# Optimization experiments

Hardware: AMD Instinct MI355X
Metric: run time of the kernel (lower is better)

The kernel has to match this reference:

```python
import jax, jax.numpy as jnp
import numpy as np

B, S, D = 8, 2048, 512

def setup_inputs() -> dict:
    key = jax.random.key(0)
    ks = jax.random.split(key, 9)
    scale = 1.0 / np.sqrt(D)
    q = jax.random.normal(ks[0], (B, S, D), dtype=jnp.float32)
    k = jax.random.normal(ks[1], (B, S, D), dtype=jnp.float32)
    v = jax.random.normal(ks[2], (B, S, D), dtype=jnp.float32)
    # causal mask, broadcast over batch: True = attend
    mask = jnp.tril(jnp.ones((S, S), dtype=bool))[None, :, :]
    Wq = jax.random.normal(ks[3], (D, D), dtype=jnp.float32) * scale
    bq = jax.random.normal(ks[4], (D,), dtype=jnp.float32) * scale
    Wk = jax.random.normal(ks[5], (D, D), dtype=jnp.float32) * scale
    bk = jax.random.normal(ks[6], (D,), dtype=jnp.float32) * scale
    Wv = jax.random.normal(ks[7], (D, D), dtype=jnp.float32) * scale
    bv = jax.random.normal(ks[8], (D,), dtype=jnp.float32) * scale
    return {"q": q, "k": k, "v": v, "mask": mask,
            "Wq": Wq, "bq": bq, "Wk": Wk, "bk": bk, "Wv": Wv, "bv": bv}

def reference(q, k, v, mask, Wq, bq, Wk, bk, Wv, bv):
    # torch nn.Linear: x @ W^T + b
    Q = jnp.einsum('bsd,ed->bse', q, Wq) + bq
    K = jnp.einsum('bsd,ed->bse', k, Wk) + bk
    V = jnp.einsum('bsd,ed->bse', v, Wv) + bv
    scores = jnp.einsum('bqd,bkd->bqk', Q, K) / jnp.sqrt(jnp.float32(D))
    scores = jnp.where(mask, scores, jnp.float32(-1e9))
    prob = jax.nn.softmax(scores, axis=-1)
    out = jnp.einsum('bqk,bkd->bqd', prob, V)
    return out
```

## Files before the change

### kernel.cpp

```cpp
#include <hip/hip_runtime.h>
#include <stdint.h>
#include <stddef.h>
#include <math.h>

typedef _Float16 half8 __attribute__((ext_vector_type(8)));
typedef float f32x4 __attribute__((ext_vector_type(4)));

#define SCALE_QK 0.04419417382415922f

__device__ __forceinline__ void gload16(const void* g, void* lds) {
  __builtin_amdgcn_global_load_lds(
      (const __attribute__((address_space(1))) void*)g,
      (__attribute__((address_space(3))) void*)lds,
      16, 0, 0);
}

template<bool A_F32>
__device__ __forceinline__ void run_kloop(const void* Arow0, const _Float16* Brow0,
                                          int lda, int ldb, int kIters,
                                          _Float16* As0, _Float16* As1,
                                          _Float16* Bs0, _Float16* Bs1,
                                          f32x4 (&acc)[4][4])
{
  const int tid  = threadIdx.x;
  const int lane = tid & 63;
  const int w    = tid >> 6;
  const int wm   = w >> 1, wn = w & 1;
  const int srow = tid >> 3;
  const int sg   = tid & 7;
  const int swz  = sg ^ (srow & 7);
  const int fr   = lane & 15;
  const int fq   = lane >> 4;
  const int fx   = lane & 7;

  f32x4 preF[8];

  auto loadAreg = [&](int it) {
    const float* A = (const float*)Arow0;
    const int k0 = it * 64;
    #pragma unroll
    for (int i = 0; i < 4; ++i) {
      const float* src = A + (size_t)(i*32 + srow) * lda + (k0 + sg*8);
      preF[2*i]   = *(const f32x4*)src;
      preF[2*i+1] = *(const f32x4*)(src + 4);
    }
  };
  auto writeA = [&](_Float16* dst) {
    #pragma unroll
    for (int i = 0; i < 4; ++i) {
      f32x4 x = preF[2*i], y = preF[2*i+1];
      half8 h;
      h[0]=(_Float16)x[0]; h[1]=(_Float16)x[1]; h[2]=(_Float16)x[2]; h[3]=(_Float16)x[3];
      h[4]=(_Float16)y[0]; h[5]=(_Float16)y[1]; h[6]=(_Float16)y[2]; h[7]=(_Float16)y[3];
      *(half8*)(dst + (i*32 + srow)*64 + swz*8) = h;
    }
  };
  auto gloadA = [&](int it, _Float16* dst) {
    const _Float16* A = (const _Float16*)Arow0;
    const int k0 = it * 64;
    #pragma unroll
    for (int i = 0; i < 4; ++i)
      gload16(A + (size_t)(i*32 + srow) * lda + (k0 + swz*8), dst + i*2048 + w*512);
  };
  auto gloadB = [&](int it, _Float16* dst) {
    const int k0 = it * 64;
    #pragma unroll
    for (int i = 0; i < 4; ++i)
      gload16(Brow0 + (size_t)(i*32 + srow) * ldb + (k0 + swz*8), dst + i*2048 + w*512);
  };
  auto stage = [&](int it, _Float16* dA, _Float16* dB) {
    if constexpr (A_F32) loadAreg(it);
    else                 gloadA(it, dA);
    gloadB(it, dB);
  };
  auto compute = [&](const _Float16* cAs, const _Float16* cBs) {
    #pragma unroll
    for (int ks = 0; ks < 2; ++ks) {
      half8 av[4], bv[4];
      const int slot = (ks*4 + fq) ^ fx;
      #pragma unroll
      for (int i = 0; i < 4; ++i) {
        av[i] = *(const half8*)(cAs + (wm*64 + i*16 + fr)*64 + slot*8);
        bv[i] = *(const half8*)(cBs + (wn*64 + i*16 + fr)*64 + slot*8);
      }
      #pragma unroll
      for (int i = 0; i < 4; ++i) {
        #pragma unroll
        for (int j = 0; j < 4; ++j)
          acc[i][j] = __builtin_amdgcn_mfma_f32_16x16x32_f16(av[i], bv[j], acc[i][j], 0, 0, 0);
      }
    }
  };

  stage(0, As0, Bs0);
  if constexpr (A_F32) writeA(As0);
  __syncthreads();

  for (int it = 0; it < kIters; it += 2) {
    stage(it + 1, As1, Bs1);
    compute(As0, Bs0);
    if constexpr (A_F32) writeA(As1);
    __syncthreads();
    const bool more = (it + 2) < kIters;
    if (more) stage(it + 2, As0, Bs0);
    compute(As1, Bs1);
    if constexpr (A_F32) { if (more) writeA(As0); }
    __syncthreads();
  }
}

__global__ __launch_bounds__(256) void k_cvtw(const float* __restrict__ Wq,
                                              const float* __restrict__ Wk,
                                              const float* __restrict__ Wv,
                                              _Float16* __restrict__ Wb)
{
  const int t = blockIdx.x * 256 + threadIdx.x;
  const int base = t * 8;
  const int z = base >> 18;
  const int off = base & 262143;
  const float* src = (z == 0) ? Wq : ((z == 1) ? Wk : Wv);
  f32x4 a = *(const f32x4*)(src + off);
  f32x4 b = *(const f32x4*)(src + off + 4);
  half8 h;
  h[0]=(_Float16)a[0]; h[1]=(_Float16)a[1]; h[2]=(_Float16)a[2]; h[3]=(_Float16)a[3];
  h[4]=(_Float16)b[0]; h[5]=(_Float16)b[1]; h[6]=(_Float16)b[2]; h[7]=(_Float16)b[3];
  *(half8*)(Wb + base) = h;
}

__global__ __launch_bounds__(256) void k_proj(const float* __restrict__ q,
                                              const float* __restrict__ k,
                                              const float* __restrict__ v,
                                              const _Float16* __restrict__ Wb,
                                              const float* __restrict__ bq,
                                              const float* __restrict__ bk,
                                              const float* __restrict__ bv,
                                              _Float16* __restrict__ Qb,
                                              _Float16* __restrict__ Kb,
                                              _Float16* __restrict__ Vb)
{
  __shared__ __align__(16) _Float16 As0[128*64], As1[128*64];
  __shared__ __align__(16) _Float16 Bs0[128*64], Bs1[128*64];
  const int bid = blockIdx.x;
  const int xcd = bid & 7, i = bid >> 3;
  const int p = xcd * 48 + (i >> 2);
  const int nt = i & 3;
  const int z = p >> 7, mt = p & 127;

  const float* A     = (z == 0) ? q  : (z == 1) ? k  : v;
  const float* bia   = (z == 0) ? bq : (z == 1) ? bk : bv;
  const _Float16* B  = Wb + (size_t)z * 512 * 512;
  _Float16* C        = (z == 0) ? Qb : (z == 1) ? Kb : Vb;

  f32x4 acc[4][4] = {};
  run_kloop<true>(A + (size_t)mt*128*512, B + (size_t)nt*128*512, 512, 512, 8,
                  As0, As1, Bs0, Bs1, acc);

  const int lane = threadIdx.x & 63, w = threadIdx.x >> 6;
  const int wm = w >> 1, wn = w & 1;
  const int fr = lane & 15, fq = lane >> 4;
  #pragma unroll
  for (int j = 0; j < 4; ++j) {
    const int col = nt*128 + wn*64 + j*16 + fr;
    const float bval = bia[col];
    #pragma unroll
    for (int i2 = 0; i2 < 4; ++i2) {
      const int row = mt*128 + wm*64 + i2*16 + fq*4;
      #pragma unroll
      for (int r = 0; r < 4; ++r)
        C[(size_t)(row + r) * 512 + col] = (_Float16)(acc[i2][j][r] + bval);
    }
  }
}

__global__ __launch_bounds__(256) void k_trans(const _Float16* __restrict__ Vb,
                                               _Float16* __restrict__ Vt)
{
  __shared__ __align__(16) _Float16 t[64][72];
  const int st = blockIdx.x, dt = blockIdx.y, b = blockIdx.z;
  const int r = threadIdx.x >> 2, g = threadIdx.x & 3;
  const _Float16* src = Vb + ((size_t)b*2048 + st*64 + r)*512 + dt*64 + g*16;
  half8 v0 = *(const half8*)src;
  half8 v1 = *(const half8*)(src + 8);
  *(half8*)&t[r][g*16]     = v0;
  *(half8*)&t[r][g*16 + 8] = v1;
  __syncthreads();
  half8 o0, o1;
  #pragma unroll
  for (int i2 = 0; i2 < 8; ++i2) o0[i2] = t[g*16 + i2][r];
  #pragma unroll
  for (int i2 = 0; i2 < 8; ++i2) o1[i2] = t[g*16 + 8 + i2][r];
  _Float16* dst = Vt + ((size_t)b*512 + dt*64 + r)*2048 + st*64 + g*16;
  *(half8*)dst       = o0;
  *(half8*)(dst + 8) = o1;
}

__global__ __launch_bounds__(256) void k_scores(const _Float16* __restrict__ Qb,
                                                const _Float16* __restrict__ Kb,
                                                _Float16* __restrict__ P)
{
  const int bid = blockIdx.x;
  const int b = bid & 7;
  const int t = bid >> 3;
  int qt = (int)((sqrtf(8.0f * (float)t + 1.0f) - 1.0f) * 0.5f);
  int base = (qt * (qt + 1)) >> 1;
  if (t < base)                { --qt; base = (qt * (qt + 1)) >> 1; }
  else if (t >= base + qt + 1) { ++qt; base = (qt * (qt + 1)) >> 1; }
  const int kt = t - base;

  __shared__ __align__(16) _Float16 As0[128*64], As1[128*64];
  __shared__ __align__(16) _Float16 Bs0[128*64], Bs1[128*64];
  f32x4 acc[4][4] = {};
  run_kloop<false>(Qb + ((size_t)b*2048 + qt*128)*512,
                   Kb + ((size_t)b*2048 + kt*128)*512,
                   512, 512, 8, As0, As1, Bs0, Bs1, acc);
  const int lane = threadIdx.x & 63, w = threadIdx.x >> 6;
  const int wm = w >> 1, wn = w & 1;
  const int fr = lane & 15, fq = lane >> 4;
  #pragma unroll
  for (int i = 0; i < 4; ++i) {
    const int row = qt*128 + wm*64 + i*16 + fq*4;
    #pragma unroll
    for (int j = 0; j < 4; ++j) {
      const int col = kt*128 + wn*64 + j*16 + fr;
      #pragma unroll
      for (int r = 0; r < 4; ++r)
        P[((size_t)b*2048 + row + r) * 2048 + col] = (_Float16)(acc[i][j][r] * SCALE_QK);
    }
  }
}

__global__ __launch_bounds__(256) void k_softmax(_Float16* __restrict__ P)
{
  const int lane = threadIdx.x & 63;
  const int row  = blockIdx.x * 4 + (threadIdx.x >> 6);
  const int qIdx = row & 2047;
  _Float16* p = P + (size_t)row * 2048;
  const int L    = qIdx + 1;
  const int Lpad = ((qIdx >> 7) + 1) * 128;

  half8 xb[4];
  float m = -1e30f, s = 0.f;
  #pragma unroll
  for (int c = 0; c < 4; ++c) {
    const int i0 = lane * 8 + c * 512;
    if (i0 < Lpad) {
      half8 x = *(const half8*)(p + i0);
      xb[c] = x;
      float xv[8];
      #pragma unroll
      for (int j = 0; j < 8; ++j) xv[j] = (i0 + j < L) ? (float)x[j] : -1e30f;
      float cm = xv[0];
      #pragma unroll
      for (int j = 1; j < 8; ++j) cm = fmaxf(cm, xv[j]);
      const float mn = fmaxf(m, cm);
      float cs = 0.f;
      #pragma unroll
      for (int j = 0; j < 8; ++j) cs += __expf(xv[j] - mn);
      s = s * __expf(m - mn) + cs;
      m = mn;
    }
  }
  #pragma unroll
  for (int d = 1; d < 64; d <<= 1) {
    const float mo = __shfl_xor(m, d, 64);
    const float so = __shfl_xor(s, d, 64);
    const float mn = fmaxf(m, mo);
    s = s * __expf(m - mn) + so * __expf(mo - mn);
    m = mn;
  }
  const float inv = 1.0f / s;

  #pragma unroll
  for (int c = 0; c < 4; ++c) {
    const int i0 = lane * 8 + c * 512;
    if (i0 < Lpad) {
      half8 x = xb[c];
      half8 o;
      #pragma unroll
      for (int j = 0; j < 8; ++j)
        o[j] = (i0 + j < L) ? (_Float16)(__expf((float)x[j] - m) * inv) : (_Float16)0.f;
      *(half8*)(p + i0) = o;
    }
  }
}

__global__ __launch_bounds__(256) void k_pv(const _Float16* __restrict__ P,
                                            const _Float16* __restrict__ Vt,
                                            float* __restrict__ Out)
{
  const int bid = blockIdx.x;
  const int b = bid & 7;
  const int r0 = bid >> 3;
  const int qi = r0 >> 2, dt = r0 & 3;
  const int qt = (qi & 1) ? (15 - (qi >> 1)) : (qi >> 1);

  __shared__ __align__(16) _Float16 As0[128*64], As1[128*64];
  __shared__ __align__(16) _Float16 Bs0[128*64], Bs1[128*64];
  f32x4 acc[4][4] = {};
  run_kloop<false>(P  + ((size_t)b*2048 + qt*128)*2048,
                   Vt + ((size_t)b*512  + dt*128)*2048,
                   2048, 2048, (qt + 1) * 2, As0, As1, Bs0, Bs1, acc);
  const int lane = threadIdx.x & 63, w = threadIdx.x >> 6;
  const int wm = w >> 1, wn = w & 1;
  const int fr = lane & 15, fq = lane >> 4;
  #pragma unroll
  for (int i = 0; i < 4; ++i) {
    const int row = qt*128 + wm*64 + i*16 + fq*4;
    #pragma unroll
    for (int j = 0; j < 4; ++j) {
      const int col = dt*128 + wn*64 + j*16 + fr;
      #pragma unroll
      for (int r = 0; r < 4; ++r)
        Out[((size_t)b*2048 + row + r) * 512 + col] = acc[i][j][r];
    }
  }
}

extern "C" void kernel_launch(void* const* d_in, const int* in_sizes, int n_in,
                              void* d_out, int out_size, void* d_ws, size_t ws_size,
                              hipStream_t stream) {
  (void)in_sizes; (void)n_in; (void)out_size;
  const float* q  = (const float*)d_in[0];
  const float* k  = (const float*)d_in[1];
  const float* v  = (const float*)d_in[2];
  const float* Wq = (const float*)d_in[4];
  const float* bq = (const float*)d_in[5];
  const float* Wk = (const float*)d_in[6];
  const float* bk = (const float*)d_in[7];
  const float* Wv = (const float*)d_in[8];
  const float* bv = (const float*)d_in[9];

  const size_t OFF_P  = 0;
  const size_t OFF_Q  = (size_t)64 << 20;
  const size_t OFF_K  = (size_t)80 << 20;
  const size_t OFF_V  = (size_t)96 << 20;
  const size_t OFF_VT = (size_t)112 << 20;
  const size_t OFF_W  = (size_t)128 << 20;
  const size_t NEEDED = OFF_W + (size_t)3 * 512 * 512 * sizeof(_Float16);
  if (ws_size < NEEDED) return;

  char* ws = (char*)d_ws;
  _Float16* P  = (_Float16*)(ws + OFF_P);
  _Float16* Qb = (_Float16*)(ws + OFF_Q);
  _Float16* Kb = (_Float16*)(ws + OFF_K);
  _Float16* Vb = (_Float16*)(ws + OFF_V);
  _Float16* Vt = (_Float16*)(ws + OFF_VT);
  _Float16* Wb = (_Float16*)(ws + OFF_W);
  float* Out = (float*)d_out;

  k_cvtw   <<<dim3(384),      dim3(256), 0, stream>>>(Wq, Wk, Wv, Wb);
  k_proj   <<<dim3(1536),     dim3(256), 0, stream>>>(q, k, v, Wb, bq, bk, bv, Qb, Kb, Vb);
  k_trans  <<<dim3(32, 8, 8), dim3(256), 0, stream>>>(Vb, Vt);
  k_scores <<<dim3(1088),     dim3(256), 0, stream>>>(Qb, Kb, P);
  k_softmax<<<dim3(4096),     dim3(256), 0, stream>>>(P);
  k_pv     <<<dim3(512),      dim3(256), 0, stream>>>(P, Vt, Out);
}
```

Measured before the change: 272.5 us.

## Deepen GEMM k-loop prefetch using explicit vmcnt waits and raw barriers

Restructures the double-buffered k-loop so two stages are in flight at once. It replaces __syncthreads with raw s_barrier plus explicit s_waitcnt vmcnt/lgkmcnt counts, so the current tile's loads are waited on while the next tile's loads stay outstanding. The aim is to hide global-load latency behind MFMA compute. In exchange it adds more barriers per iteration, and correctness now depends on hand-counted vmcnt values matching the number of issued loads.

```diff
diff --git a/kernel.cpp b/kernel.cpp
--- a/kernel.cpp
+++ b/kernel.cpp
@@ -7,6 +7,11 @@
 typedef float f32x4 __attribute__((ext_vector_type(4)));
 
 #define SCALE_QK 0.04419417382415922f
+
+#define WAITVM(N) asm volatile("s_waitcnt vmcnt(" #N ")" ::: "memory")
+#define WAITLG0() asm volatile("s_waitcnt lgkmcnt(0)" ::: "memory")
+#define BAR()     __builtin_amdgcn_s_barrier()
+#define SCHED0()  __builtin_amdgcn_sched_barrier(0)
 
 __device__ __forceinline__ void gload16(const void* g, void* lds) {
   __builtin_amdgcn_global_load_lds(
@@ -92,20 +97,46 @@
     }
   };
 
-  stage(0, As0, Bs0);
-  if constexpr (A_F32) writeA(As0);
-  __syncthreads();
+  if constexpr (A_F32) {
+    loadAreg(0);
+    gloadB(0, Bs0);
+    writeA(As0);
+    loadAreg(1);
+    gloadB(1, Bs1);
+    WAITVM(12);
+    WAITLG0();
+  } else {
+    gloadA(0, As0); gloadB(0, Bs0);
+    gloadA(1, As1); gloadB(1, Bs1);
+    WAITVM(8);
+  }
+  BAR();
+  SCHED0();
 
   for (int it = 0; it < kIters; it += 2) {
-    stage(it + 1, As1, Bs1);
+    const bool more = (it + 2) < kIters;
+
     compute(As0, Bs0);
-    if constexpr (A_F32) writeA(As1);
-    __syncthreads();
-    const bool more = (it + 2) < kIters;
-    if (more) stage(it + 2, As0, Bs0);
+    if constexpr (A_F32) { writeA(As1); WAITLG0(); }
+    BAR();
+    if (more) {
+      stage(it + 2, As0, Bs0);
+      if constexpr (A_F32) { WAITVM(12); } else { WAITVM(8); }
+    } else {
+      WAITVM(0);
+    }
+    BAR();
+    SCHED0();
+
     compute(As1, Bs1);
-    if constexpr (A_F32) { if (more) writeA(As0); }
-    __syncthreads();
+    if (more) {
+      if constexpr (A_F32) { writeA(As0); WAITLG0(); }
+      BAR();
+      stage(it + 3, As1, Bs1);
+      if constexpr (A_F32) { WAITVM(12); } else { WAITVM(8); }
+      BAR();
+      SCHED0();
+    }
   }
 }
 
```

New measurement: 276.1 us. About the same (+1.3%).

## Fuse softmax into score and PV kernels and fuse V transpose into projection

Applied to the files above, without the earlier changes.

The score kernel now computes per-tile row max and exp-sum and stores them alongside the raw scaled scores. The PV kernel merges these tile statistics into a global row max and reciprocal sum, applies exp on the fly to the P fragments before the MFMA, and normalizes the output. This removes the separate softmax pass over P. The V projection epilogue also writes its result transposed through LDS, so the separate transpose kernel is gone. The cost is extra exp work in the PV inner loop, recomputed once per d-tile, and added reductions and syncs in the score epilogue.

```diff
diff --git a/kernel.cpp b/kernel.cpp
--- a/kernel.cpp
+++ b/kernel.cpp
@@ -15,12 +15,12 @@
       16, 0, 0);
 }
 
-template<bool A_F32>
+template<bool A_F32, bool EXPA>
 __device__ __forceinline__ void run_kloop(const void* Arow0, const _Float16* Brow0,
                                           int lda, int ldb, int kIters,
                                           _Float16* As0, _Float16* As1,
                                           _Float16* Bs0, _Float16* Bs1,
-                                          f32x4 (&acc)[4][4])
+                                          f32x4 (&acc)[4][4], const float (&mr)[4])
 {
   const int tid  = threadIdx.x;
   const int lane = tid & 63;
@@ -82,6 +82,14 @@
       for (int i = 0; i < 4; ++i) {
         av[i] = *(const half8*)(cAs + (wm*64 + i*16 + fr)*64 + slot*8);
         bv[i] = *(const half8*)(cBs + (wn*64 + i*16 + fr)*64 + slot*8);
+      }
+      if constexpr (EXPA) {
+        #pragma unroll
+        for (int i = 0; i < 4; ++i) {
+          #pragma unroll
+          for (int e = 0; e < 8; ++e)
+            av[i][e] = (_Float16)__expf((float)av[i][e] - mr[i]);
+        }
       }
       #pragma unroll
       for (int i = 0; i < 4; ++i) {
@@ -136,10 +144,14 @@
                                               const float* __restrict__ bv,
                                               _Float16* __restrict__ Qb,
                                               _Float16* __restrict__ Kb,
-                                              _Float16* __restrict__ Vb)
+                                              _Float16* __restrict__ Vt)
 {
-  __shared__ __align__(16) _Float16 As0[128*64], As1[128*64];
-  __shared__ __align__(16) _Float16 Bs0[128*64], Bs1[128*64];
+  __shared__ __align__(16) _Float16 LDSbuf[4*128*64];
+  _Float16* As0 = LDSbuf;
+  _Float16* As1 = LDSbuf + 8192;
+  _Float16* Bs0 = LDSbuf + 16384;
+  _Float16* Bs1 = LDSbuf + 24576;
+
   const int bid = blockIdx.x;
   const int xcd = bid & 7, i = bid >> 3;
   const int p = xcd * 48 + (i >> 2);
@@ -149,55 +161,69 @@
   const float* A     = (z == 0) ? q  : (z == 1) ? k  : v;
   const float* bia   = (z == 0) ? bq : (z == 1) ? bk : bv;
   const _Float16* B  = Wb + (size_t)z * 512 * 512;
-  _Float16* C        = (z == 0) ? Qb : (z == 1) ? Kb : Vb;
 
   f32x4 acc[4][4] = {};
-  run_kloop<true>(A + (size_t)mt*128*512, B + (size_t)nt*128*512, 512, 512, 8,
-                  As0, As1, Bs0, Bs1, acc);
-
-  const int lane = threadIdx.x & 63, w = threadIdx.x >> 6;
+  const float mrd[4] = {0,0,0,0};
+  run_kloop<true, false>(A + (size_t)mt*128*512, B + (size_t)nt*128*512, 512, 512, 8,
+                         As0, As1, Bs0, Bs1, acc, mrd);
+
+  const int tid = threadIdx.x;
+  const int lane = tid & 63, w = tid >> 6;
   const int wm = w >> 1, wn = w & 1;
   const int fr = lane & 15, fq = lane >> 4;
-  #pragma unroll
-  for (int j = 0; j < 4; ++j) {
-    const int col = nt*128 + wn*64 + j*16 + fr;
-    const float bval = bia[col];
-    #pragma unroll
-    for (int i2 = 0; i2 < 4; ++i2) {
-      const int row = mt*128 + wm*64 + i2*16 + fq*4;
-      #pragma unroll
-      for (int r = 0; r < 4; ++r)
-        C[(size_t)(row + r) * 512 + col] = (_Float16)(acc[i2][j][r] + bval);
-    }
-  }
-}
-
-__global__ __launch_bounds__(256) void k_trans(const _Float16* __restrict__ Vb,
-                                               _Float16* __restrict__ Vt)
-{
-  __shared__ __align__(16) _Float16 t[64][72];
-  const int st = blockIdx.x, dt = blockIdx.y, b = blockIdx.z;
-  const int r = threadIdx.x >> 2, g = threadIdx.x & 3;
-  const _Float16* src = Vb + ((size_t)b*2048 + st*64 + r)*512 + dt*64 + g*16;
-  half8 v0 = *(const half8*)src;
-  half8 v1 = *(const half8*)(src + 8);
-  *(half8*)&t[r][g*16]     = v0;
-  *(half8*)&t[r][g*16 + 8] = v1;
-  __syncthreads();
-  half8 o0, o1;
-  #pragma unroll
-  for (int i2 = 0; i2 < 8; ++i2) o0[i2] = t[g*16 + i2][r];
-  #pragma unroll
-  for (int i2 = 0; i2 < 8; ++i2) o1[i2] = t[g*16 + 8 + i2][r];
-  _Float16* dst = Vt + ((size_t)b*512 + dt*64 + r)*2048 + st*64 + g*16;
-  *(half8*)dst       = o0;
-  *(half8*)(dst + 8) = o1;
+
+  if (z < 2) {
+    _Float16* C = (z == 0) ? Qb : Kb;
+    #pragma unroll
+    for (int j = 0; j < 4; ++j) {
+      const int col = nt*128 + wn*64 + j*16 + fr;
+      const float bval = bia[col];
+      #pragma unroll
+      for (int i2 = 0; i2 < 4; ++i2) {
+        const int row = mt*128 + wm*64 + i2*16 + fq*4;
+        #pragma unroll
+        for (int r = 0; r < 4; ++r)
+          C[(size_t)(row + r) * 512 + col] = (_Float16)(acc[i2][j][r] + bval);
+      }
+    }
+  } else {
+    _Float16* sm = LDSbuf;
+    #pragma unroll
+    for (int j = 0; j < 4; ++j) {
+      const int colloc = wn*64 + j*16 + fr;
+      const float bval = bia[nt*128 + colloc];
+      #pragma unroll
+      for (int i2 = 0; i2 < 4; ++i2) {
+        const int rowloc = wm*64 + i2*16 + fq*4;
+        #pragma unroll
+        for (int r = 0; r < 4; ++r)
+          sm[colloc*136 + rowloc + r] = (_Float16)(acc[i2][j][r] + bval);
+      }
+    }
+    __syncthreads();
+    const int bb = mt >> 4, s0 = (mt & 15) * 128;
+    #pragma unroll
+    for (int q8 = 0; q8 < 8; ++q8) {
+      const int dloc = q8*16 + (tid >> 4);
+      const int ch   = tid & 15;
+      half8 o = *(const half8*)&sm[dloc*136 + ch*8];
+      *(half8*)(Vt + ((size_t)bb*512 + nt*128 + dloc)*2048 + s0 + ch*8) = o;
+    }
+  }
 }
 
 __global__ __launch_bounds__(256) void k_scores(const _Float16* __restrict__ Qb,
                                                 const _Float16* __restrict__ Kb,
-                                                _Float16* __restrict__ P)
+                                                _Float16* __restrict__ P,
+                                                float* __restrict__ Sm,
+                                                float* __restrict__ Sl)
 {
+  __shared__ __align__(16) _Float16 LDSbuf[4*128*64];
+  _Float16* As0 = LDSbuf;
+  _Float16* As1 = LDSbuf + 8192;
+  _Float16* Bs0 = LDSbuf + 16384;
+  _Float16* Bs1 = LDSbuf + 24576;
+
   const int bid = blockIdx.x;
   const int b = bid & 7;
   const int t = bid >> 3;
@@ -206,103 +232,144 @@
   if (t < base)                { --qt; base = (qt * (qt + 1)) >> 1; }
   else if (t >= base + qt + 1) { ++qt; base = (qt * (qt + 1)) >> 1; }
   const int kt = t - base;
-
-  __shared__ __align__(16) _Float16 As0[128*64], As1[128*64];
-  __shared__ __align__(16) _Float16 Bs0[128*64], Bs1[128*64];
+  const bool diag = (kt == qt);
+
   f32x4 acc[4][4] = {};
-  run_kloop<false>(Qb + ((size_t)b*2048 + qt*128)*512,
-                   Kb + ((size_t)b*2048 + kt*128)*512,
-                   512, 512, 8, As0, As1, Bs0, Bs1, acc);
-  const int lane = threadIdx.x & 63, w = threadIdx.x >> 6;
+  const float mrd[4] = {0,0,0,0};
+  run_kloop<false, false>(Qb + ((size_t)b*2048 + qt*128)*512,
+                          Kb + ((size_t)b*2048 + kt*128)*512,
+                          512, 512, 8, As0, As1, Bs0, Bs1, acc, mrd);
+
+  const int tid = threadIdx.x;
+  const int lane = tid & 63, w = tid >> 6;
   const int wm = w >> 1, wn = w & 1;
   const int fr = lane & 15, fq = lane >> 4;
+
+  float* sf = (float*)LDSbuf;
+  float rmax[4][4];
   #pragma unroll
   for (int i = 0; i < 4; ++i) {
-    const int row = qt*128 + wm*64 + i*16 + fq*4;
+    #pragma unroll
+    for (int r = 0; r < 4; ++r) {
+      const int rl = wm*64 + i*16 + fq*4 + r;
+      float v = -1e30f;
+      #pragma unroll
+      for (int j = 0; j < 4; ++j) {
+        const int cl = wn*64 + j*16 + fr;
+        const float sc = acc[i][j][r] * SCALE_QK;
+        v = fmaxf(v, (diag && cl > rl) ? -1e30f : sc);
+      }
+      #pragma unroll
+      for (int d = 1; d < 16; d <<= 1) v = fmaxf(v, __shfl_xor(v, d, 64));
+      rmax[i][r] = v;
+      if (fr == 0) sf[wn*128 + rl] = v;
+    }
+  }
+  __syncthreads();
+  float M[4][4];
+  #pragma unroll
+  for (int i = 0; i < 4; ++i)
+    #pragma unroll
+    for (int r = 0; r < 4; ++r) {
+      const int rl = wm*64 + i*16 + fq*4 + r;
+      M[i][r] = fmaxf(sf[rl], sf[128 + rl]);
+    }
+  #pragma unroll
+  for (int i = 0; i < 4; ++i) {
+    #pragma unroll
+    for (int r = 0; r < 4; ++r) {
+      const int rl = wm*64 + i*16 + fq*4 + r;
+      float sacc = 0.f;
+      #pragma unroll
+      for (int j = 0; j < 4; ++j) {
+        const int cl = wn*64 + j*16 + fr;
+        const float sc = acc[i][j][r] * SCALE_QK;
+        const float se = (diag && cl > rl) ? -1e30f : sc;
+        sacc += __expf(se - M[i][r]);
+      }
+      #pragma unroll
+      for (int d = 1; d < 16; d <<= 1) sacc += __shfl_xor(sacc, d, 64);
+      if (fr == 0) sf[256 + wn*128 + rl] = sacc;
+    }
+  }
+  __syncthreads();
+  if (wn == 0 && fr == 0) {
+    const size_t sbase = (size_t)((b*16 + qt)*16 + kt) * 128;
+    #pragma unroll
+    for (int i = 0; i < 4; ++i)
+      #pragma unroll
+      for (int r = 0; r < 4; ++r) {
+        const int rl = wm*64 + i*16 + fq*4 + r;
+        Sm[sbase + rl] = M[i][r];
+        Sl[sbase + rl] = sf[256 + rl] + sf[384 + rl];
+      }
+  }
+
+  #pragma unroll
+  for (int i = 0; i < 4; ++i) {
+    const int rl = wm*64 + i*16 + fq*4;
     #pragma unroll
     for (int j = 0; j < 4; ++j) {
-      const int col = kt*128 + wn*64 + j*16 + fr;
-      #pragma unroll
-      for (int r = 0; r < 4; ++r)
-        P[((size_t)b*2048 + row + r) * 2048 + col] = (_Float16)(acc[i][j][r] * SCALE_QK);
-    }
-  }
-}
-
-__global__ __launch_bounds__(256) void k_softmax(_Float16* __restrict__ P)
-{
-  const int lane = threadIdx.x & 63;
-  const int row  = blockIdx.x * 4 + (threadIdx.x >> 6);
-  const int qIdx = row & 2047;
-  _Float16* p = P + (size_t)row * 2048;
-  const int L    = qIdx + 1;
-  const int Lpad = ((qIdx >> 7) + 1) * 128;
-
-  half8 xb[4];
-  float m = -1e30f, s = 0.f;
-  #pragma unroll
-  for (int c = 0; c < 4; ++c) {
-    const int i0 = lane * 8 + c * 512;
-    if (i0 < Lpad) {
-      half8 x = *(const half8*)(p + i0);
-      xb[c] = x;
-      float xv[8];
-      #pragma unroll
-      for (int j = 0; j < 8; ++j) xv[j] = (i0 + j < L) ? (float)x[j] : -1e30f;
-      float cm = xv[0];
-      #pragma unroll
-      for (int j = 1; j < 8; ++j) cm = fmaxf(cm, xv[j]);
-      const float mn = fmaxf(m, cm);
-      float cs = 0.f;
-      #pragma unroll
-      for (int j = 0; j < 8; ++j) cs += __expf(xv[j] - mn);
-      s = s * __expf(m - mn) + cs;
-      m = mn;
-    }
-  }
-  #pragma unroll
-  for (int d = 1; d < 64; d <<= 1) {
-    const float mo = __shfl_xor(m, d, 64);
-    const float so = __shfl_xor(s, d, 64);
-    const float mn = fmaxf(m, mo);
-    s = s * __expf(m - mn) + so * __expf(mo - mn);
-    m = mn;
-  }
-  const float inv = 1.0f / s;
-
-  #pragma unroll
-  for (int c = 0; c < 4; ++c) {
-    const int i0 = lane * 8 + c * 512;
-    if (i0 < Lpad) {
-      half8 x = xb[c];
-      half8 o;
-      #pragma unroll
-      for (int j = 0; j < 8; ++j)
-        o[j] = (i0 + j < L) ? (_Float16)(__expf((float)x[j] - m) * inv) : (_Float16)0.f;
-      *(half8*)(p + i0) = o;
+      const int cl = wn*64 + j*16 + fr;
+      #pragma unroll
+      for (int r = 0; r < 4; ++r) {
+        const float sc = acc[i][j][r] * SCALE_QK;
+        const bool msk = diag && (cl > rl + r);
+        P[((size_t)b*2048 + qt*128 + rl + r) * 2048 + kt*128 + cl] =
+            msk ? (_Float16)(-30000.0f) : (_Float16)sc;
+      }
     }
   }
 }
 
 __global__ __launch_bounds__(256) void k_pv(const _Float16* __restrict__ P,
+                                            const float* __restrict__ Sm,
+                                            const float* __restrict__ Sl,
                                             const _Float16* __restrict__ Vt,
                                             float* __restrict__ Out)
 {
+  __shared__ __align__(16) _Float16 LDSbuf[4*128*64];
+  _Float16* As0 = LDSbuf;
+  _Float16* As1 = LDSbuf + 8192;
+  _Float16* Bs0 = LDSbuf + 16384;
+  _Float16* Bs1 = LDSbuf + 24576;
+
   const int bid = blockIdx.x;
   const int b = bid & 7;
   const int r0 = bid >> 3;
   const int qi = r0 >> 2, dt = r0 & 3;
   const int qt = (qi & 1) ? (15 - (qi >> 1)) : (qi >> 1);
 
-  __shared__ __align__(16) _Float16 As0[128*64], As1[128*64];
-  __shared__ __align__(16) _Float16 Bs0[128*64], Bs1[128*64];
-  f32x4 acc[4][4] = {};
-  run_kloop<false>(P  + ((size_t)b*2048 + qt*128)*2048,
-                   Vt + ((size_t)b*512  + dt*128)*2048,
-                   2048, 2048, (qt + 1) * 2, As0, As1, Bs0, Bs1, acc);
-  const int lane = threadIdx.x & 63, w = threadIdx.x >> 6;
+  const int tid = threadIdx.x;
+  const int lane = tid & 63, w = tid >> 6;
   const int wm = w >> 1, wn = w & 1;
   const int fr = lane & 15, fq = lane >> 4;
+
+  float* tmp = (float*)LDSbuf;
+  const size_t sbase = (size_t)((b*16 + qt)*16) * 128;
+  if (tid < 128) {
+    float m = -1e30f;
+    for (int kt = 0; kt <= qt; ++kt) m = fmaxf(m, Sm[sbase + kt*128 + tid]);
+    float l = 0.f;
+    for (int kt = 0; kt <= qt; ++kt)
+      l += Sl[sbase + kt*128 + tid] * __expf(Sm[sbase + kt*128 + tid] - m);
+    tmp[tid] = m;
+    tmp[128 + tid] = 1.0f / l;
+  }
+  __syncthreads();
+  float mr[4];
+  f32x4 il[4];
+  #pragma unroll
+  for (int i = 0; i < 4; ++i) mr[i] = tmp[wm*64 + i*16 + fr];
+  #pragma unroll
+  for (int i = 0; i < 4; ++i) il[i] = *(const f32x4*)&tmp[128 + wm*64 + i*16 + fq*4];
+  __syncthreads();
+
+  f32x4 acc[4][4] = {};
+  run_kloop<false, true>(P  + ((size_t)b*2048 + qt*128)*2048,
+                         Vt + ((size_t)b*512  + dt*128)*2048,
+                         2048, 2048, (qt + 1) * 2, As0, As1, Bs0, Bs1, acc, mr);
+
   #pragma unroll
   for (int i = 0; i < 4; ++i) {
     const int row = qt*128 + wm*64 + i*16 + fq*4;
@@ -311,7 +378,7 @@
       const int col = dt*128 + wn*64 + j*16 + fr;
       #pragma unroll
       for (int r = 0; r < 4; ++r)
-        Out[((size_t)b*2048 + row + r) * 512 + col] = acc[i][j][r];
+        Out[((size_t)b*2048 + row + r) * 512 + col] = acc[i][j][r] * il[i][r];
     }
   }
 }
@@ -333,7 +400,8 @@
   const size_t OFF_P  = 0;
   const size_t OFF_Q  = (size_t)64 << 20;
   const size_t OFF_K  = (size_t)80 << 20;
-  const size_t OFF_V  = (size_t)96 << 20;
+  const size_t OFF_SM = (size_t)96 << 20;
+  const size_t OFF_SL = (size_t)98 << 20;
   const size_t OFF_VT = (size_t)112 << 20;
   const size_t OFF_W  = (size_t)128 << 20;
   const size_t NEEDED = OFF_W + (size_t)3 * 512 * 512 * sizeof(_Float16);
@@ -343,15 +411,14 @@
   _Float16* P  = (_Float16*)(ws + OFF_P);
   _Float16* Qb = (_Float16*)(ws + OFF_Q);
   _Float16* Kb = (_Float16*)(ws + OFF_K);
-  _Float16* Vb = (_Float16*)(ws + OFF_V);
+  float*    Sm = (float*)(ws + OFF_SM);
+  float*    Sl = (float*)(ws + OFF_SL);
   _Float16* Vt = (_Float16*)(ws + OFF_VT);
   _Float16* Wb = (_Float16*)(ws + OFF_W);
   float* Out = (float*)d_out;
 
-  k_cvtw   <<<dim3(384),      dim3(256), 0, stream>>>(Wq, Wk, Wv, Wb);
-  k_proj   <<<dim3(1536),     dim3(256), 0, stream>>>(q, k, v, Wb, bq, bk, bv, Qb, Kb, Vb);
-  k_trans  <<<dim3(32, 8, 8), dim3(256), 0, stream>>>(Vb, Vt);
-  k_scores <<<dim3(1088),     dim3(256), 0, stream>>>(Qb, Kb, P);
-  k_softmax<<<dim3(4096),     dim3(256), 0, stream>>>(P);
-  k_pv     <<<dim3(512),      dim3(256), 0, stream>>>(P, Vt, Out);
-}
+  k_cvtw   <<<dim3(384),  dim3(256), 0, stream>>>(Wq, Wk, Wv, Wb);
+  k_proj   <<<dim3(1536), dim3(256), 0, stream>>>(q, k, v, Wb, bq, bk, bv, Qb, Kb, Vt);
+  k_scores <<<dim3(1088), dim3(256), 0, stream>>>(Qb, Kb, P, Sm, Sl);
+  k_pv     <<<dim3(512),  dim3(256), 0, stream>>>(P, Sm, Sl, Vt, Out);
+}
```

Result: slower. 296.5 us (+8.8%).

## Fuse V transpose into projection and use 128x256 tiles with direct-global A operand

Applied to the files above, without the earlier changes.

The V projection epilogue now transposes through LDS and writes Vt directly, which removes the separate transpose kernel and the Vb round trip. The scores and PV kernels switch to 128x256 output tiles. Their A operand (Q or P) is read straight from global memory into registers instead of staged in LDS, and only B is double-buffered in LDS. Scores blocks cover pairs of key tiles, with the masked diagonal written as a large negative value. This halves the block counts and raises per-block reuse, at the cost of more registers (launch_bounds 2), uncoalesced direct A loads, and wasted compute on pairs that extend past the diagonal.

```diff
diff --git a/kernel.cpp b/kernel.cpp
--- a/kernel.cpp
+++ b/kernel.cpp
@@ -15,12 +15,11 @@
       16, 0, 0);
 }
 
-template<bool A_F32>
-__device__ __forceinline__ void run_kloop(const void* Arow0, const _Float16* Brow0,
-                                          int lda, int ldb, int kIters,
-                                          _Float16* As0, _Float16* As1,
-                                          _Float16* Bs0, _Float16* Bs1,
-                                          f32x4 (&acc)[4][4])
+__device__ __forceinline__ void run_kloop_proj(const float* Arow0, const _Float16* Brow0,
+                                               int lda, int ldb, int kIters,
+                                               _Float16* As0, _Float16* As1,
+                                               _Float16* Bs0, _Float16* Bs1,
+                                               f32x4 (&acc)[4][4])
 {
   const int tid  = threadIdx.x;
   const int lane = tid & 63;
@@ -36,11 +35,10 @@
   f32x4 preF[8];
 
   auto loadAreg = [&](int it) {
-    const float* A = (const float*)Arow0;
     const int k0 = it * 64;
     #pragma unroll
     for (int i = 0; i < 4; ++i) {
-      const float* src = A + (size_t)(i*32 + srow) * lda + (k0 + sg*8);
+      const float* src = Arow0 + (size_t)(i*32 + srow) * lda + (k0 + sg*8);
       preF[2*i]   = *(const f32x4*)src;
       preF[2*i+1] = *(const f32x4*)(src + 4);
     }
@@ -55,23 +53,11 @@
       *(half8*)(dst + (i*32 + srow)*64 + swz*8) = h;
     }
   };
-  auto gloadA = [&](int it, _Float16* dst) {
-    const _Float16* A = (const _Float16*)Arow0;
-    const int k0 = it * 64;
-    #pragma unroll
-    for (int i = 0; i < 4; ++i)
-      gload16(A + (size_t)(i*32 + srow) * lda + (k0 + swz*8), dst + i*2048 + w*512);
-  };
   auto gloadB = [&](int it, _Float16* dst) {
     const int k0 = it * 64;
     #pragma unroll
     for (int i = 0; i < 4; ++i)
       gload16(Brow0 + (size_t)(i*32 + srow) * ldb + (k0 + swz*8), dst + i*2048 + w*512);
-  };
-  auto stage = [&](int it, _Float16* dA, _Float16* dB) {
-    if constexpr (A_F32) loadAreg(it);
-    else                 gloadA(it, dA);
-    gloadB(it, dB);
   };
   auto compute = [&](const _Float16* cAs, const _Float16* cBs) {
     #pragma unroll
@@ -92,19 +78,79 @@
     }
   };
 
-  stage(0, As0, Bs0);
-  if constexpr (A_F32) writeA(As0);
+  loadAreg(0);
+  gloadB(0, Bs0);
+  writeA(As0);
   __syncthreads();
 
   for (int it = 0; it < kIters; it += 2) {
-    stage(it + 1, As1, Bs1);
+    loadAreg(it + 1);
+    gloadB(it + 1, Bs1);
     compute(As0, Bs0);
-    if constexpr (A_F32) writeA(As1);
+    writeA(As1);
     __syncthreads();
     const bool more = (it + 2) < kIters;
-    if (more) stage(it + 2, As0, Bs0);
+    if (more) { loadAreg(it + 2); gloadB(it + 2, Bs0); }
     compute(As1, Bs1);
-    if constexpr (A_F32) { if (more) writeA(As0); }
+    if (more) writeA(As0);
+    __syncthreads();
+  }
+}
+
+__device__ __forceinline__ void run_kloop_dA(const _Float16* Arow0, const _Float16* Brow0,
+                                             int lda, int ldb, int kIters,
+                                             _Float16* Bs0, _Float16* Bs1,
+                                             f32x4 (&acc)[4][8])
+{
+  const int tid  = threadIdx.x;
+  const int lane = tid & 63;
+  const int w    = tid >> 6;
+  const int wm   = w >> 1, wn = w & 1;
+  const int srow = tid >> 3;
+  const int sg   = tid & 7;
+  const int swz  = sg ^ (srow & 7);
+  const int fr   = lane & 15;
+  const int fq   = lane >> 4;
+  const int fx   = lane & 7;
+
+  auto stageB = [&](int it, _Float16* dst) {
+    const int k0 = it * 64;
+    #pragma unroll
+    for (int i = 0; i < 8; ++i)
+      gload16(Brow0 + (size_t)(i*32 + srow) * ldb + (k0 + swz*8), dst + i*2048 + w*512);
+  };
+  auto compute = [&](const _Float16* cBs, int it) {
+    const int k0 = it * 64;
+    half8 av[2][4];
+    #pragma unroll
+    for (int ks = 0; ks < 2; ++ks)
+      #pragma unroll
+      for (int i = 0; i < 4; ++i)
+        av[ks][i] = *(const half8*)(Arow0 + (size_t)(wm*64 + i*16 + fr)*lda + k0 + ks*32 + fq*8);
+    #pragma unroll
+    for (int ks = 0; ks < 2; ++ks) {
+      half8 bv[8];
+      const int slot = (ks*4 + fq) ^ fx;
+      #pragma unroll
+      for (int j = 0; j < 8; ++j)
+        bv[j] = *(const half8*)(cBs + (wn*128 + j*16 + fr)*64 + slot*8);
+      #pragma unroll
+      for (int i = 0; i < 4; ++i)
+        #pragma unroll
+        for (int j = 0; j < 8; ++j)
+          acc[i][j] = __builtin_amdgcn_mfma_f32_16x16x32_f16(av[ks][i], bv[j], acc[i][j], 0, 0, 0);
+    }
+  };
+
+  stageB(0, Bs0);
+  __syncthreads();
+  for (int it = 0; it < kIters; it += 2) {
+    stageB(it + 1, Bs1);
+    compute(Bs0, it);
+    __syncthreads();
+    const bool more = (it + 2) < kIters;
+    if (more) stageB(it + 2, Bs0);
+    compute(Bs1, it + 1);
     __syncthreads();
   }
 }
@@ -136,10 +182,14 @@
                                               const float* __restrict__ bv,
                                               _Float16* __restrict__ Qb,
                                               _Float16* __restrict__ Kb,
-                                              _Float16* __restrict__ Vb)
-{
-  __shared__ __align__(16) _Float16 As0[128*64], As1[128*64];
-  __shared__ __align__(16) _Float16 Bs0[128*64], Bs1[128*64];
+                                              _Float16* __restrict__ Vt)
+{
+  __shared__ __align__(16) _Float16 LDSbuf[4*128*64];
+  _Float16* As0 = LDSbuf;
+  _Float16* As1 = LDSbuf + 8192;
+  _Float16* Bs0 = LDSbuf + 16384;
+  _Float16* Bs1 = LDSbuf + 24576;
+
   const int bid = blockIdx.x;
   const int xcd = bid & 7, i = bid >> 3;
   const int p = xcd * 48 + (i >> 2);
@@ -149,82 +199,96 @@
   const float* A     = (z == 0) ? q  : (z == 1) ? k  : v;
   const float* bia   = (z == 0) ? bq : (z == 1) ? bk : bv;
   const _Float16* B  = Wb + (size_t)z * 512 * 512;
-  _Float16* C        = (z == 0) ? Qb : (z == 1) ? Kb : Vb;
 
   f32x4 acc[4][4] = {};
-  run_kloop<true>(A + (size_t)mt*128*512, B + (size_t)nt*128*512, 512, 512, 8,
-                  As0, As1, Bs0, Bs1, acc);
-
-  const int lane = threadIdx.x & 63, w = threadIdx.x >> 6;
+  run_kloop_proj(A + (size_t)mt*128*512, B + (size_t)nt*128*512, 512, 512, 8,
+                 As0, As1, Bs0, Bs1, acc);
+
+  const int tid = threadIdx.x;
+  const int lane = tid & 63, w = tid >> 6;
   const int wm = w >> 1, wn = w & 1;
   const int fr = lane & 15, fq = lane >> 4;
-  #pragma unroll
-  for (int j = 0; j < 4; ++j) {
-    const int col = nt*128 + wn*64 + j*16 + fr;
-    const float bval = bia[col];
-    #pragma unroll
-    for (int i2 = 0; i2 < 4; ++i2) {
-      const int row = mt*128 + wm*64 + i2*16 + fq*4;
-      #pragma unroll
-      for (int r = 0; r < 4; ++r)
-        C[(size_t)(row + r) * 512 + col] = (_Float16)(acc[i2][j][r] + bval);
-    }
-  }
-}
-
-__global__ __launch_bounds__(256) void k_trans(const _Float16* __restrict__ Vb,
-                                               _Float16* __restrict__ Vt)
-{
-  __shared__ __align__(16) _Float16 t[64][72];
-  const int st = blockIdx.x, dt = blockIdx.y, b = blockIdx.z;
-  const int r = threadIdx.x >> 2, g = threadIdx.x & 3;
-  const _Float16* src = Vb + ((size_t)b*2048 + st*64 + r)*512 + dt*64 + g*16;
-  half8 v0 = *(const half8*)src;
-  half8 v1 = *(const half8*)(src + 8);
-  *(half8*)&t[r][g*16]     = v0;
-  *(half8*)&t[r][g*16 + 8] = v1;
-  __syncthreads();
-  half8 o0, o1;
-  #pragma unroll
-  for (int i2 = 0; i2 < 8; ++i2) o0[i2] = t[g*16 + i2][r];
-  #pragma unroll
-  for (int i2 = 0; i2 < 8; ++i2) o1[i2] = t[g*16 + 8 + i2][r];
-  _Float16* dst = Vt + ((size_t)b*512 + dt*64 + r)*2048 + st*64 + g*16;
-  *(half8*)dst       = o0;
-  *(half8*)(dst + 8) = o1;
-}
-
-__global__ __launch_bounds__(256) void k_scores(const _Float16* __restrict__ Qb,
-                                                const _Float16* __restrict__ Kb,
-                                                _Float16* __restrict__ P)
-{
+
+  if (z < 2) {
+    _Float16* C = (z == 0) ? Qb : Kb;
+    #pragma unroll
+    for (int j = 0; j < 4; ++j) {
+      const int col = nt*128 + wn*64 + j*16 + fr;
+      const float bval = bia[col];
+      #pragma unroll
+      for (int i2 = 0; i2 < 4; ++i2) {
+        const int row = mt*128 + wm*64 + i2*16 + fq*4;
+        #pragma unroll
+        for (int r = 0; r < 4; ++r)
+          C[(size_t)(row + r) * 512 + col] = (_Float16)(acc[i2][j][r] + bval);
+      }
+    }
+  } else {
+    _Float16* sm = LDSbuf;
+    #pragma unroll
+    for (int j = 0; j < 4; ++j) {
+      const int colloc = wn*64 + j*16 + fr;
+      const float bval = bia[nt*128 + colloc];
+      #pragma unroll
+      for (int i2 = 0; i2 < 4; ++i2) {
+        const int rowloc = wm*64 + i2*16 + fq*4;
+        #pragma unroll
+        for (int r = 0; r < 4; ++r)
+          sm[colloc*136 + rowloc + r] = (_Float16)(acc[i2][j][r] + bval);
+      }
+    }
+    __syncthreads();
+    const int bb = mt >> 4, s0 = (mt & 15) * 128;
+    #pragma unroll
+    for (int q8 = 0; q8 < 8; ++q8) {
+      const int dloc = q8*16 + (tid >> 4);
+      const int ch   = tid & 15;
+      half8 o = *(const half8*)&sm[dloc*136 + ch*8];
+      *(half8*)(Vt + ((size_t)bb*512 + nt*128 + dloc)*2048 + s0 + ch*8) = o;
+    }
+  }
+}
+
+__global__ __launch_bounds__(256, 2) void k_scores(const _Float16* __restrict__ Qb,
+                                                   const _Float16* __restrict__ Kb,
+                                                   _Float16* __restrict__ P)
+{
+  __shared__ __align__(16) _Float16 Bs0[256*64], Bs1[256*64];
   const int bid = blockIdx.x;
   const int b = bid & 7;
-  const int t = bid >> 3;
-  int qt = (int)((sqrtf(8.0f * (float)t + 1.0f) - 1.0f) * 0.5f);
-  int base = (qt * (qt + 1)) >> 1;
-  if (t < base)                { --qt; base = (qt * (qt + 1)) >> 1; }
-  else if (t >= base + qt + 1) { ++qt; base = (qt * (qt + 1)) >> 1; }
-  const int kt = t - base;
-
-  __shared__ __align__(16) _Float16 As0[128*64], As1[128*64];
-  __shared__ __align__(16) _Float16 Bs0[128*64], Bs1[128*64];
-  f32x4 acc[4][4] = {};
-  run_kloop<false>(Qb + ((size_t)b*2048 + qt*128)*512,
-                   Kb + ((size_t)b*2048 + kt*128)*512,
-                   512, 512, 8, As0, As1, Bs0, Bs1, acc);
-  const int lane = threadIdx.x & 63, w = threadIdx.x >> 6;
+  const int t = 71 - (bid >> 3);
+  int qt = 0, accum = 0;
+  while (accum + (qt/2 + 1) <= t) { accum += qt/2 + 1; ++qt; }
+  const int kt2 = t - accum;
+  const int kt0 = kt2 * 2;
+
+  f32x4 acc[4][8] = {};
+  run_kloop_dA(Qb + ((size_t)b*2048 + qt*128)*512,
+               Kb + ((size_t)b*2048 + kt0*128)*512,
+               512, 512, 8, Bs0, Bs1, acc);
+
+  const int tid = threadIdx.x;
+  const int lane = tid & 63, w = tid >> 6;
   const int wm = w >> 1, wn = w & 1;
   const int fr = lane & 15, fq = lane >> 4;
-  #pragma unroll
-  for (int i = 0; i < 4; ++i) {
-    const int row = qt*128 + wm*64 + i*16 + fq*4;
-    #pragma unroll
-    for (int j = 0; j < 4; ++j) {
-      const int col = kt*128 + wn*64 + j*16 + fr;
-      #pragma unroll
-      for (int r = 0; r < 4; ++r)
-        P[((size_t)b*2048 + row + r) * 2048 + col] = (_Float16)(acc[i][j][r] * SCALE_QK);
+
+  const int kt = kt0 + wn;
+  if (kt <= qt) {
+    const bool diag = (kt == qt);
+    #pragma unroll
+    for (int i = 0; i < 4; ++i) {
+      const int rl = wm*64 + i*16 + fq*4;
+      #pragma unroll
+      for (int j = 0; j < 8; ++j) {
+        const int cl = j*16 + fr;
+        #pragma unroll
+        for (int r = 0; r < 4; ++r) {
+          const float sc = acc[i][j][r] * SCALE_QK;
+          const bool msk = diag && (cl > rl + r);
+          P[((size_t)b*2048 + qt*128 + rl + r) * 2048 + kt*128 + cl] =
+              msk ? (_Float16)(-30000.0f) : (_Float16)sc;
+        }
+      }
     }
   }
 }
@@ -284,31 +348,32 @@
   }
 }
 
-__global__ __launch_bounds__(256) void k_pv(const _Float16* __restrict__ P,
-                                            const _Float16* __restrict__ Vt,
-                                            float* __restrict__ Out)
-{
+__global__ __launch_bounds__(256, 2) void k_pv(const _Float16* __restrict__ P,
+                                               const _Float16* __restrict__ Vt,
+                                               float* __restrict__ Out)
+{
+  __shared__ __align__(16) _Float16 Bs0[256*64], Bs1[256*64];
   const int bid = blockIdx.x;
   const int b = bid & 7;
   const int r0 = bid >> 3;
-  const int qi = r0 >> 2, dt = r0 & 3;
+  const int qi = r0 >> 1, dt2 = r0 & 1;
   const int qt = (qi & 1) ? (15 - (qi >> 1)) : (qi >> 1);
 
-  __shared__ __align__(16) _Float16 As0[128*64], As1[128*64];
-  __shared__ __align__(16) _Float16 Bs0[128*64], Bs1[128*64];
-  f32x4 acc[4][4] = {};
-  run_kloop<false>(P  + ((size_t)b*2048 + qt*128)*2048,
-                   Vt + ((size_t)b*512  + dt*128)*2048,
-                   2048, 2048, (qt + 1) * 2, As0, As1, Bs0, Bs1, acc);
-  const int lane = threadIdx.x & 63, w = threadIdx.x >> 6;
+  f32x4 acc[4][8] = {};
+  run_kloop_dA(P  + ((size_t)b*2048 + qt*128)*2048,
+               Vt + ((size_t)b*512  + dt2*256)*2048,
+               2048, 2048, (qt + 1) * 2, Bs0, Bs1, acc);
+
+  const int tid = threadIdx.x;
+  const int lane = tid & 63, w = tid >> 6;
   const int wm = w >> 1, wn = w & 1;
   const int fr = lane & 15, fq = lane >> 4;
   #pragma unroll
   for (int i = 0; i < 4; ++i) {
     const int row = qt*128 + wm*64 + i*16 + fq*4;
     #pragma unroll
-    for (int j = 0; j < 4; ++j) {
-      const int col = dt*128 + wn*64 + j*16 + fr;
+    for (int j = 0; j < 8; ++j) {
+      const int col = dt2*256 + wn*128 + j*16 + fr;
       #pragma unroll
       for (int r = 0; r < 4; ++r)
         Out[((size_t)b*2048 + row + r) * 512 + col] = acc[i][j][r];
@@ -333,7 +398,6 @@
   const size_t OFF_P  = 0;
   const size_t OFF_Q  = (size_t)64 << 20;
   const size_t OFF_K  = (size_t)80 << 20;
-  const size_t OFF_V  = (size_t)96 << 20;
   const size_t OFF_VT = (size_t)112 << 20;
   const size_t OFF_W  = (size_t)128 << 20;
   const size_t NEEDED = OFF_W + (size_t)3 * 512 * 512 * sizeof(_Float16);
@@ -343,15 +407,13 @@
   _Float16* P  = (_Float16*)(ws + OFF_P);
   _Float16* Qb = (_Float16*)(ws + OFF_Q);
   _Float16* Kb = (_Float16*)(ws + OFF_K);
-  _Float16* Vb = (_Float16*)(ws + OFF_V);
   _Float16* Vt = (_Float16*)(ws + OFF_VT);
   _Float16* Wb = (_Float16*)(ws + OFF_W);
   float* Out = (float*)d_out;
 
-  k_cvtw   <<<dim3(384),      dim3(256), 0, stream>>>(Wq, Wk, Wv, Wb);
-  k_proj   <<<dim3(1536),     dim3(256), 0, stream>>>(q, k, v, Wb, bq, bk, bv, Qb, Kb, Vb);
-  k_trans  <<<dim3(32, 8, 8), dim3(256), 0, stream>>>(Vb, Vt);
-  k_scores <<<dim3(1088),     dim3(256), 0, stream>>>(Qb, Kb, P);
-  k_softmax<<<dim3(4096),     dim3(256), 0, stream>>>(P);
-  k_pv     <<<dim3(512),      dim3(256), 0, stream>>>(P, Vt, Out);
-}
+  k_cvtw   <<<dim3(384),  dim3(256), 0, stream>>>(Wq, Wk, Wv, Wb);
+  k_proj   <<<dim3(1536), dim3(256), 0, stream>>>(q, k, v, Wb, bq, bk, bv, Qb, Kb, Vt);
+  k_scores <<<dim3(576),  dim3(256), 0, stream>>>(Qb, Kb, P);
+  k_softmax<<<dim3(4096), dim3(256), 0, stream>>>(P);
+  k_pv     <<<dim3(256),  dim3(256), 0, stream>>>(P, Vt, Out);
+}
```

Result: slower. 360.0 us (+32.1%).
